# Optimization experiments

Measured on AMD Instinct MI355X. Metric: run time of the kernel, lower is better.

## Reference

```python
import jax, jax.numpy as jnp
import numpy as np

D_MODEL = 1024
NUM_HEADS = 16
DEPTH = D_MODEL // NUM_HEADS  # 64
BATCH, SEQ = 4, 2048


def setup_inputs() -> dict:
    key = jax.random.key(0)
    ks = jax.random.split(key, 9)
    s = 1.0 / np.sqrt(D_MODEL)
    x = jax.random.normal(ks[0], (BATCH, SEQ, D_MODEL), dtype=jnp.float32)
    # Per-head Dense weights stacked on a leading head axis [H, d_model, depth]
    Wq = jax.random.normal(ks[1], (NUM_HEADS, D_MODEL, DEPTH), dtype=jnp.float32) * s
    Wk = jax.random.normal(ks[2], (NUM_HEADS, D_MODEL, DEPTH), dtype=jnp.float32) * s
    Wv = jax.random.normal(ks[3], (NUM_HEADS, D_MODEL, DEPTH), dtype=jnp.float32) * s
    bq = jnp.zeros((NUM_HEADS, DEPTH), dtype=jnp.float32)
    bk = jnp.zeros((NUM_HEADS, DEPTH), dtype=jnp.float32)
    bv = jnp.zeros((NUM_HEADS, DEPTH), dtype=jnp.float32)
    Wo = jax.random.normal(ks[4], (D_MODEL, D_MODEL), dtype=jnp.float32) * s
    bo = jnp.zeros((D_MODEL,), dtype=jnp.float32)
    return {"x": x, "Wq": Wq, "bq": bq, "Wk": Wk, "bk": bk,
            "Wv": Wv, "bv": bv, "Wo": Wo, "bo": bo}


def reference(x, Wq, bq, Wk, bk, Wv, bv, Wo, bo):
    # Batched equivalent of the per-head loop: project, attend, concat heads.
    q = jnp.einsum('bsd,hde->bhse', x, Wq) + bq[:, None, :]  # [B,H,S,depth]
    k = jnp.einsum('bsd,hde->bhse', x, Wk) + bk[:, None, :]
    v = jnp.einsum('bsd,hde->bhse', x, Wv) + bv[:, None, :]
    scale = 1.0 / jnp.sqrt(jnp.asarray(DEPTH, dtype=x.dtype))
    scores = jnp.einsum('bhse,bhte->bhst', q, k) * scale      # [B,H,S,S]
    weights = jax.nn.softmax(scores, axis=-1)
    heads = jnp.einsum('bhst,bhte->bhse', weights, v)         # [B,H,S,depth]
    # concat head outputs along last axis in head order (tf.concat axis=-1)
    multi = jnp.transpose(heads, (0, 2, 1, 3)).reshape(x.shape[0], x.shape[1], D_MODEL)
    return multi @ Wo + bo
```

## Files before the change

kernel.cpp:

```cpp
#include <hip/hip_runtime.h>
#include <hip/hip_bf16.h>

#define BATCH 4
#define SEQ   2048
#define DM    1024
#define NH    16
#define DEPTH 64
#define ROWS  (BATCH*SEQ)
#define NQKV  (3*DM)
#define BH    (BATCH*NH)

typedef __attribute__((ext_vector_type(8))) short bf16x8;
typedef __attribute__((ext_vector_type(4))) float f32x4;
typedef __attribute__((ext_vector_type(16))) float f32x16;
typedef unsigned short u16;
typedef unsigned int   u32;

__device__ __forceinline__ u16 f2bf(float f) {
    union { float f; unsigned u; } v; v.f = f;
    unsigned r = v.u + 0x7fff + ((v.u >> 16) & 1);
    return (u16)(r >> 16);
}

__device__ __forceinline__ u32 pk2bf(float a, float b) {
#if __has_builtin(__builtin_amdgcn_cvt_pk_bf16_f32)
    typedef __attribute__((ext_vector_type(2))) __bf16 v2bf;
    union { v2bf v; u32 u; } u_;
    u_.v = __builtin_amdgcn_cvt_pk_bf16_f32(a, b);
    return u_.u;
#else
    return (u32)f2bf(a) | ((u32)f2bf(b) << 16);
#endif
}

__device__ __forceinline__ void plswap(u32 a, u32 b, u32& x, u32& y) {
#if __has_builtin(__builtin_amdgcn_permlane32_swap)
    typedef __attribute__((ext_vector_type(2))) int i32x2;
    i32x2 r = __builtin_amdgcn_permlane32_swap((int)a, (int)b, false, false);
    x = (u32)r.x; y = (u32)r.y;
#else
    u32 as = (u32)__shfl_xor((int)a, 32);
    u32 bs = (u32)__shfl_xor((int)b, 32);
    int h = (threadIdx.x >> 5) & 1;
    x = h ? bs : a;
    y = h ? b : as;
#endif
}

__device__ __forceinline__ void g2l16(void* lds, const void* g) {
    __builtin_amdgcn_global_load_lds((const __attribute__((address_space(1))) void*)g,
                                     (__attribute__((address_space(3))) void*)lds, 16, 0, 0);
}

__device__ __forceinline__ bf16x8 frag8(const u16* tile, int row, int gl) {
    return *(const bf16x8*)(tile + row * 64 + ((gl ^ (row & 7)) * 8));
}

__device__ __forceinline__ f32x16 mfma32(bf16x8 a, bf16x8 b, f32x16 c) {
    return __builtin_amdgcn_mfma_f32_32x32x16_bf16(a, b, c, 0, 0, 0);
}

__global__ __launch_bounds__(256) void k_prep(const float* __restrict__ x,
                                              const float* __restrict__ Wq, const float* __restrict__ Wk,
                                              const float* __restrict__ Wv, const float* __restrict__ Wo,
                                              u16* __restrict__ xb, u16* __restrict__ BT, u16* __restrict__ WoT) {
    __shared__ u16 T[64][65];
    int tid = threadIdx.x;
    int bx = blockIdx.x;
    if (bx < 2048) {
        int i = bx * 4096 + tid * 4;
        for (int l = 0; l < 4; ++l) {
            float4 v = *(const float4*)(x + i + l * 1024);
            ushort4 o; o.x = f2bf(v.x); o.y = f2bf(v.y); o.z = f2bf(v.z); o.w = f2bf(v.w);
            *(ushort4*)(xb + i + l * 1024) = o;
        }
        return;
    }
    if (bx < 2816) {
        int q = bx - 2048;
        int kt = q & 15, mh = q >> 4, m = mh >> 4, h = mh & 15;
        const float* W = (m == 0) ? Wq : (m == 1) ? Wk : Wv;
        const float* src = W + ((size_t)h * 1024 + kt * 64) * 64;
        int e = tid & 63, r0 = tid >> 6;
        for (int i = 0; i < 16; ++i) { int r = i * 4 + r0; T[r][e] = f2bf(src[r * 64 + e]); }
        __syncthreads();
        int kk = tid & 63, e0 = tid >> 6;
        u16* dst = BT + ((size_t)m * 1024 + h * 64) * 1024 + kt * 64;
        for (int i = 0; i < 16; ++i) { int ee = i * 4 + e0; dst[ee * 1024 + kk] = T[kk][ee]; }
        return;
    }
    {
        int q = bx - 2816;
        int kt = q & 15, nt = q >> 4;
        const float* src = Wo + (size_t)kt * 64 * 1024 + nt * 64;
        int c = tid & 63, r0 = tid >> 6;
        for (int i = 0; i < 16; ++i) { int r = i * 4 + r0; T[r][c] = f2bf(src[r * 1024 + c]); }
        __syncthreads();
        int kk = tid & 63, e0 = tid >> 6;
        u16* dst = WoT + (size_t)nt * 64 * 1024 + kt * 64;
        for (int i = 0; i < 16; ++i) { int ee = i * 4 + e0; dst[ee * 1024 + kk] = T[kk][ee]; }
    }
}

__global__ __launch_bounds__(256, 2) void k_gemm_qkv(const u16* __restrict__ xb, const u16* __restrict__ Wt,
                                                     const float* __restrict__ bq, const float* __restrict__ bk,
                                                     const float* __restrict__ bv,
                                                     u16* __restrict__ Q, u16* __restrict__ K, u16* __restrict__ VT) {
    __shared__ u16 Al[2][128 * 64];
    __shared__ u16 Bl[2][128 * 64];
    int tid = threadIdx.x;
    int wave = tid >> 6, lane = tid & 63, l31 = lane & 31, h2 = lane >> 5;
    int wr = wave >> 1, wc = wave & 1;

    int b = blockIdx.x;
    int wg = (b & 7) * 192 + (b >> 3);

    bool isvt = (wg >= 1024);
    int row0, col0;
    const u16 *Am, *Bm;
    if (!isvt) {
        row0 = (wg >> 4) * 128; col0 = (wg & 15) * 128;
        Am = xb + (size_t)row0 * 1024;
        Bm = Wt + (size_t)col0 * 1024;
    } else {
        int b2 = wg - 1024;
        row0 = (b2 >> 6) * 128; col0 = (b2 & 63) * 128;
        Am = Wt + (size_t)(2048 + row0) * 1024;
        Bm = xb + (size_t)col0 * 1024;
    }

    f32x16 acc[2][2] = {};

    int sr[4], sgs[4], sdst[4];
#pragma unroll
    for (int l = 0; l < 4; ++l) {
        int idx = tid + l * 256;
        sr[l] = idx >> 3; sgs[l] = ((idx & 7) ^ (sr[l] & 7)) * 8; sdst[l] = idx * 8;
    }

#define QKV_STAGE(bufi, k0) \
    { _Pragma("unroll") for (int l = 0; l < 4; ++l) { \
        g2l16(&Al[bufi][sdst[l]], Am + sr[l] * 1024 + (k0) + sgs[l]); \
        g2l16(&Bl[bufi][sdst[l]], Bm + sr[l] * 1024 + (k0) + sgs[l]); } }

#define QKV_COMPUTE(bufi) \
    { _Pragma("unroll") for (int kk = 0; kk < 4; ++kk) { \
        bf16x8 a_[2], bb_[2]; \
        _Pragma("unroll") for (int mi = 0; mi < 2; ++mi) a_[mi] = frag8(Al[bufi], wr * 64 + mi * 32 + l31, 2 * kk + h2); \
        _Pragma("unroll") for (int ni = 0; ni < 2; ++ni) bb_[ni] = frag8(Bl[bufi], wc * 64 + ni * 32 + l31, 2 * kk + h2); \
        _Pragma("unroll") for (int mi = 0; mi < 2; ++mi) \
        _Pragma("unroll") for (int ni = 0; ni < 2; ++ni) \
            acc[mi][ni] = mfma32(a_[mi], bb_[ni], acc[mi][ni]); } }

    QKV_STAGE(0, 0)
    QKV_STAGE(1, 64)

    for (int t = 0; t < 15; ++t) {
        int cur = t & 1;
        asm volatile("s_waitcnt vmcnt(8)" ::: "memory");
        __builtin_amdgcn_s_barrier();
        asm volatile("" ::: "memory");
        __builtin_amdgcn_s_setprio(1);
        QKV_COMPUTE(cur)
        __builtin_amdgcn_s_setprio(0);
        asm volatile("" ::: "memory");
        __builtin_amdgcn_s_barrier();
        if (t < 14) QKV_STAGE(cur, (t + 2) * 64)
    }
    asm volatile("s_waitcnt vmcnt(0)" ::: "memory");
    __builtin_amdgcn_s_barrier();
    asm volatile("" ::: "memory");
    QKV_COMPUTE(1)
#undef QKV_STAGE
#undef QKV_COMPUTE

    if (!isvt) {
        const float QSCALE = 0.125f * 1.4426950408889634f;
        int m = (col0 >= 1024);
        const float* bias = m ? bk : bq;
        u16* dst0 = m ? K : Q;
#pragma unroll
        for (int ni = 0; ni < 2; ++ni) {
            int c = col0 + wc * 64 + ni * 32 + l31;
            int h = (c >> 6) & 15, e = c & 63;
            float bval = bias[h * 64 + e];
#pragma unroll
            for (int mi = 0; mi < 2; ++mi)
#pragma unroll
                for (int reg = 0; reg < 16; ++reg) {
                    int rowg = row0 + wr * 64 + mi * 32 + (reg & 3) + 8 * (reg >> 2) + 4 * h2;
                    int b_ = rowg >> 11, s = rowg & 2047;
                    int bh = b_ * 16 + h;
                    float v = acc[mi][ni][reg] + bval;
                    if (!m) v *= QSCALE;
                    dst0[((size_t)bh * 2048 + s) * 64 + e] = f2bf(v);
                }
        }
    } else {
#pragma unroll
        for (int ni = 0; ni < 2; ++ni) {
            int c = col0 + wc * 64 + ni * 32 + l31;
            int b_ = c >> 11, s = c & 2047;
#pragma unroll
            for (int mi = 0; mi < 2; ++mi)
#pragma unroll
                for (int reg = 0; reg < 16; ++reg) {
                    int ii = row0 + wr * 64 + mi * 32 + (reg & 3) + 8 * (reg >> 2) + 4 * h2;
                    float v = acc[mi][ni][reg] + bv[ii];
                    VT[((size_t)b_ * 1024 + ii) * 2048 + s] = f2bf(v);
                }
        }
    }
}

__global__ __launch_bounds__(256, 4) void k_attn(const u16* __restrict__ Q, const u16* __restrict__ K,
                                                 const u16* __restrict__ VT, u16* __restrict__ A2) {
    __shared__ u16 Kl[2][64 * 64];
    __shared__ u16 Vl[3][64 * 64];
    int tid = threadIdx.x;
    int wave = tid >> 6, lane = tid & 63, l31 = lane & 31, h = lane >> 5;
    int i = blockIdx.x;
    int bh = (i & 7) * 8 + ((i >> 3) & 7);
    int m0 = (i >> 6) * 128;
    const u16* Qb = Q + (size_t)bh * 2048 * 64;
    const u16* Kb = K + (size_t)bh * 2048 * 64;
    const u16* Vb = VT + (size_t)bh * 64 * 2048;

    const u16* kp[2]; const u16* vp[2]; int dsti[2];
    for (int l = 0; l < 2; ++l) {
        int idx = tid + l * 256, r = idx >> 3, gs = ((idx & 7) ^ (r & 7)) * 8;
        dsti[l] = idx * 8;
        kp[l] = Kb + r * 64 + gs;
        vp[l] = Vb + r * 2048 + gs;
    }

    bf16x8 qb[4];
    {
        const u16* q0 = Qb + (size_t)(m0 + wave * 32 + l31) * 64 + h * 8;
#pragma unroll
        for (int s = 0; s < 4; ++s) qb[s] = *(const bf16x8*)(q0 + s * 16);
    }

    for (int l = 0; l < 2; ++l) { g2l16(&Kl[0][dsti[l]], kp[l]); g2l16(&Vl[0][dsti[l]], vp[l]); }
    asm volatile("s_waitcnt vmcnt(0)" ::: "memory");
    __builtin_amdgcn_s_barrier();
    asm volatile("" ::: "memory");

    f32x16 oacc[2] = {};
    float lsum = 0.f;
    bf16x8 pa[4] = {};
    int vw = 1;
    int vr = 2;

    for (int t = 0; t < 32; ++t) {
        int cur = t & 1, nxt = cur ^ 1;

        if (t < 31) {
            for (int l = 0; l < 2; ++l) {
                g2l16(&Kl[nxt][dsti[l]], kp[l] + (t + 1) * 4096);
                g2l16(&Vl[vw][dsti[l]], vp[l] + (t + 1) * 64);
            }
        }

        f32x16 sc[2] = {};
        __builtin_amdgcn_s_setprio(1);
#pragma unroll
        for (int s = 0; s < 4; ++s) {
            bf16x8 kf0 = frag8(Kl[cur], l31,      2 * s + h);
            bf16x8 kf1 = frag8(Kl[cur], 32 + l31, 2 * s + h);
            sc[0] = mfma32(kf0, qb[s], sc[0]);
            sc[1] = mfma32(kf1, qb[s], sc[1]);
        }
        if (t > 0) {
            const u16* vt_ = Vl[vr];
#pragma unroll
            for (int s = 0; s < 4; ++s) {
                bf16x8 bv0 = frag8(vt_, l31,      2 * s + h);
                bf16x8 bv1 = frag8(vt_, 32 + l31, 2 * s + h);
                oacc[0] = mfma32(pa[s], bv0, oacc[0]);
                oacc[1] = mfma32(pa[s], bv1, oacc[1]);
            }
        }
        __builtin_amdgcn_s_setprio(0);

        float sq = 0.f;
#pragma unroll
        for (int kt = 0; kt < 2; ++kt)
#pragma unroll
            for (int gp = 0; gp < 2; ++gp) {
                float e00 = __builtin_amdgcn_exp2f(sc[kt][(2 * gp) * 4 + 0]);
                float e01 = __builtin_amdgcn_exp2f(sc[kt][(2 * gp) * 4 + 1]);
                float e02 = __builtin_amdgcn_exp2f(sc[kt][(2 * gp) * 4 + 2]);
                float e03 = __builtin_amdgcn_exp2f(sc[kt][(2 * gp) * 4 + 3]);
                float e10 = __builtin_amdgcn_exp2f(sc[kt][(2 * gp + 1) * 4 + 0]);
                float e11 = __builtin_amdgcn_exp2f(sc[kt][(2 * gp + 1) * 4 + 1]);
                float e12 = __builtin_amdgcn_exp2f(sc[kt][(2 * gp + 1) * 4 + 2]);
                float e13 = __builtin_amdgcn_exp2f(sc[kt][(2 * gp + 1) * 4 + 3]);
                sq += ((e00 + e01) + (e02 + e03)) + ((e10 + e11) + (e12 + e13));
                u32 ue = pk2bf(e00, e01), ve = pk2bf(e02, e03);
                u32 uo = pk2bf(e10, e11), vo = pk2bf(e12, e13);
                u32 w0, w1, w2, w3;
                plswap(ue, uo, w0, w2);
                plswap(ve, vo, w1, w3);
                union { bf16x8 v; u32 w[4]; } pu;
                pu.w[0] = w0; pu.w[1] = w1; pu.w[2] = w2; pu.w[3] = w3;
                pa[2 * kt + gp] = pu.v;
            }
        lsum += sq;

        if (t < 31) {
            asm volatile("s_waitcnt vmcnt(0)" ::: "memory");
            __builtin_amdgcn_s_barrier();
            asm volatile("" ::: "memory");
        }
        vw = (vw == 2) ? 0 : vw + 1;
        vr = (vr == 2) ? 0 : vr + 1;
    }

#pragma unroll
    for (int s = 0; s < 4; ++s) {
        bf16x8 bv0 = frag8(Vl[1], l31,      2 * s + h);
        bf16x8 bv1 = frag8(Vl[1], 32 + l31, 2 * s + h);
        oacc[0] = mfma32(pa[s], bv0, oacc[0]);
        oacc[1] = mfma32(pa[s], bv1, oacc[1]);
    }

    float linv_own;
    {
        float l2 = lsum + __shfl_xor(lsum, 32);
        linv_own = 1.0f / l2;
    }
    int b_ = bh >> 4, hh = bh & 15;
    for (int g = 0; g < 4; ++g) {
#pragma unroll
        for (int r = 0; r < 4; ++r) {
            float iv = __shfl(linv_own, 8 * g + 4 * h + r);
            int row = b_ * 2048 + m0 + wave * 32 + 8 * g + 4 * h + r;
            for (int dt = 0; dt < 2; ++dt)
                A2[row * 1024 + hh * 64 + dt * 32 + l31] = f2bf(oacc[dt][g * 4 + r] * iv);
        }
    }
}

__global__ __launch_bounds__(256, 2) void k_gemm_out(const u16* __restrict__ A, const u16* __restrict__ BT,
                                                     const float* __restrict__ bo, float* __restrict__ out) {
    __shared__ u16 Al[2][128 * 64];
    __shared__ u16 Bl[2][128 * 64];
    int tid = threadIdx.x;
    int wave = tid >> 6, lane = tid & 63, l31 = lane & 31, h2 = lane >> 5;
    int wr = wave >> 1, wc = wave & 1;

    int b = blockIdx.x;
    int wg = (b & 7) * 64 + (b >> 3);
    int row0 = (wg >> 3) * 128, col0 = (wg & 7) * 128;

    const u16* Am = A  + (size_t)row0 * 1024;
    const u16* Bm = BT + (size_t)col0 * 1024;

    f32x16 acc[2][2] = {};

    int sr[4], sgs[4], sdst[4];
#pragma unroll
    for (int l = 0; l < 4; ++l) {
        int idx = tid + l * 256;
        sr[l] = idx >> 3; sgs[l] = ((idx & 7) ^ (sr[l] & 7)) * 8; sdst[l] = idx * 8;
    }

#define OUT_STAGE(bufi, k0) \
    { _Pragma("unroll") for (int l = 0; l < 4; ++l) { \
        g2l16(&Al[bufi][sdst[l]], Am + sr[l] * 1024 + (k0) + sgs[l]); \
        g2l16(&Bl[bufi][sdst[l]], Bm + sr[l] * 1024 + (k0) + sgs[l]); } }

#define OUT_COMPUTE(bufi) \
    { _Pragma("unroll") for (int kk = 0; kk < 4; ++kk) { \
        bf16x8 a_[2], bb_[2]; \
        _Pragma("unroll") for (int mi = 0; mi < 2; ++mi) a_[mi] = frag8(Al[bufi], wr * 64 + mi * 32 + l31, 2 * kk + h2); \
        _Pragma("unroll") for (int ni = 0; ni < 2; ++ni) bb_[ni] = frag8(Bl[bufi], wc * 64 + ni * 32 + l31, 2 * kk + h2); \
        _Pragma("unroll") for (int mi = 0; mi < 2; ++mi) \
        _Pragma("unroll") for (int ni = 0; ni < 2; ++ni) \
            acc[mi][ni] = mfma32(a_[mi], bb_[ni], acc[mi][ni]); } }

    OUT_STAGE(0, 0)
    OUT_STAGE(1, 64)

    for (int t = 0; t < 15; ++t) {
        int cur = t & 1;
        asm volatile("s_waitcnt vmcnt(8)" ::: "memory");
        __builtin_amdgcn_s_barrier();
        asm volatile("" ::: "memory");
        __builtin_amdgcn_s_setprio(1);
        OUT_COMPUTE(cur)
        __builtin_amdgcn_s_setprio(0);
        asm volatile("" ::: "memory");
        __builtin_amdgcn_s_barrier();
        if (t < 14) OUT_STAGE(cur, (t + 2) * 64)
    }
    asm volatile("s_waitcnt vmcnt(0)" ::: "memory");
    __builtin_amdgcn_s_barrier();
    asm volatile("" ::: "memory");
    OUT_COMPUTE(1)
#undef OUT_STAGE
#undef OUT_COMPUTE

#pragma unroll
    for (int ni = 0; ni < 2; ++ni) {
        int c = col0 + wc * 64 + ni * 32 + l31;
        float bias = bo[c];
#pragma unroll
        for (int mi = 0; mi < 2; ++mi)
#pragma unroll
            for (int reg = 0; reg < 16; ++reg) {
                int rowg = row0 + wr * 64 + mi * 32 + (reg & 3) + 8 * (reg >> 2) + 4 * h2;
                out[(size_t)rowg * 1024 + c] = acc[mi][ni][reg] + bias;
            }
    }
}

extern "C" void kernel_launch(void* const* d_in, const int* in_sizes, int n_in,
                              void* d_out, int out_size, void* d_ws, size_t ws_size,
                              hipStream_t stream) {
    const float* x  = (const float*)d_in[0];
    const float* Wq = (const float*)d_in[1];
    const float* bq = (const float*)d_in[2];
    const float* Wk = (const float*)d_in[3];
    const float* bk = (const float*)d_in[4];
    const float* Wv = (const float*)d_in[5];
    const float* bv = (const float*)d_in[6];
    const float* Wo = (const float*)d_in[7];
    const float* bo = (const float*)d_in[8];
    float* out = (float*)d_out;

    char* ws = (char*)d_ws;
    u16* xb    = (u16*)ws; ws += (size_t)ROWS * DM * 2;
    u16* WqkvT = (u16*)ws; ws += (size_t)NQKV * DM * 2;
    u16* WoT   = (u16*)ws; ws += (size_t)DM * DM * 2;
    u16* Qb    = (u16*)ws; ws += (size_t)BH * SEQ * DEPTH * 2;
    u16* Kb    = (u16*)ws; ws += (size_t)BH * SEQ * DEPTH * 2;
    u16* VTb   = (u16*)ws; ws += (size_t)BH * SEQ * DEPTH * 2;
    u16* A2    = xb;
    (void)ws_size;

    k_prep     <<<dim3(3072),   dim3(256), 0, stream>>>(x, Wq, Wk, Wv, Wo, xb, WqkvT, WoT);
    k_gemm_qkv <<<dim3(1536),   dim3(256), 0, stream>>>(xb, WqkvT, bq, bk, bv, Qb, Kb, VTb);
    k_attn     <<<dim3(1024),   dim3(256), 0, stream>>>(Qb, Kb, VTb, A2);
    k_gemm_out <<<dim3(512),    dim3(256), 0, stream>>>(A2, WoT, bo, out);
}
```

Baseline: 285.5 us.

## Unroll attention loop with static buffer indices and compute row sums via MFMA

Peels the first and last iterations of the attention K/V loop and fully unrolls the middle into six-step bodies, so LDS buffer indices are compile-time constants and the per-iteration branches and modulo-3 counters go away. The softmax denominator is now accumulated by an extra MFMA of the probability fragments against a ones vector, replacing the scalar VALU additions and the cross-lane shuffle at the end. This trades VALU work for one extra MFMA per step (about 50% more PV MFMAs) and sums the bf16-rounded probabilities, which also makes the normalization match the values used for PV. It raises code size and accumulator register pressure.

```diff
diff --git a/kernel.cpp b/kernel.cpp
--- a/kernel.cpp
+++ b/kernel.cpp
@@ -226,12 +226,12 @@
     const u16* Kb = K + (size_t)bh * 2048 * 64;
     const u16* Vb = VT + (size_t)bh * 64 * 2048;
 
-    const u16* kp[2]; const u16* vp[2]; int dsti[2];
+    const u16* kpc[2]; const u16* vpc[2]; int dsti[2];
     for (int l = 0; l < 2; ++l) {
         int idx = tid + l * 256, r = idx >> 3, gs = ((idx & 7) ^ (r & 7)) * 8;
         dsti[l] = idx * 8;
-        kp[l] = Kb + r * 64 + gs;
-        vp[l] = Vb + r * 2048 + gs;
+        kpc[l] = Kb + r * 64 + gs;
+        vpc[l] = Vb + r * 2048 + gs;
     }
 
     bf16x8 qb[4];
@@ -241,80 +241,122 @@
         for (int s = 0; s < 4; ++s) qb[s] = *(const bf16x8*)(q0 + s * 16);
     }
 
-    for (int l = 0; l < 2; ++l) { g2l16(&Kl[0][dsti[l]], kp[l]); g2l16(&Vl[0][dsti[l]], vp[l]); }
+    bf16x8 ones;
+    {
+        union { short s[8]; bf16x8 v; } o_;
+#pragma unroll
+        for (int j = 0; j < 8; ++j) o_.s[j] = (short)0x3F80;
+        ones = o_.v;
+    }
+
+    for (int l = 0; l < 2; ++l) { g2l16(&Kl[0][dsti[l]], kpc[l]); g2l16(&Vl[0][dsti[l]], vpc[l]); }
     asm volatile("s_waitcnt vmcnt(0)" ::: "memory");
     __builtin_amdgcn_s_barrier();
     asm volatile("" ::: "memory");
+    kpc[0] += 4096; kpc[1] += 4096; vpc[0] += 64; vpc[1] += 64;
 
     f32x16 oacc[2] = {};
-    float lsum = 0.f;
-    bf16x8 pa[4] = {};
-    int vw = 1;
-    int vr = 2;
-
-    for (int t = 0; t < 32; ++t) {
-        int cur = t & 1, nxt = cur ^ 1;
-
-        if (t < 31) {
-            for (int l = 0; l < 2; ++l) {
-                g2l16(&Kl[nxt][dsti[l]], kp[l] + (t + 1) * 4096);
-                g2l16(&Vl[vw][dsti[l]], vp[l] + (t + 1) * 64);
-            }
-        }
-
-        f32x16 sc[2] = {};
+    f32x16 lacc = {};
+    bf16x8 pa[4];
+
+#define ATT_EXP(sc0_, sc1_) \
+    { _Pragma("unroll") for (int kt = 0; kt < 2; ++kt) { \
+        const f32x16& s_ = kt ? (sc1_) : (sc0_); \
+        _Pragma("unroll") for (int gp = 0; gp < 2; ++gp) { \
+            float e00 = __builtin_amdgcn_exp2f(s_[(2 * gp) * 4 + 0]); \
+            float e01 = __builtin_amdgcn_exp2f(s_[(2 * gp) * 4 + 1]); \
+            float e02 = __builtin_amdgcn_exp2f(s_[(2 * gp) * 4 + 2]); \
+            float e03 = __builtin_amdgcn_exp2f(s_[(2 * gp) * 4 + 3]); \
+            float e10 = __builtin_amdgcn_exp2f(s_[(2 * gp + 1) * 4 + 0]); \
+            float e11 = __builtin_amdgcn_exp2f(s_[(2 * gp + 1) * 4 + 1]); \
+            float e12 = __builtin_amdgcn_exp2f(s_[(2 * gp + 1) * 4 + 2]); \
+            float e13 = __builtin_amdgcn_exp2f(s_[(2 * gp + 1) * 4 + 3]); \
+            u32 ue = pk2bf(e00, e01), ve = pk2bf(e02, e03); \
+            u32 uo = pk2bf(e10, e11), vo = pk2bf(e12, e13); \
+            u32 w0, w1, w2, w3; \
+            plswap(ue, uo, w0, w2); \
+            plswap(ve, vo, w1, w3); \
+            union { bf16x8 v; u32 w[4]; } pu; \
+            pu.w[0] = w0; pu.w[1] = w1; pu.w[2] = w2; pu.w[3] = w3; \
+            pa[2 * kt + gp] = pu.v; \
+        } } }
+
+#define ATT_BODY(KS, KN, VW, VR) \
+    { \
+        g2l16(&Kl[KN][dsti[0]], kpc[0]); g2l16(&Vl[VW][dsti[0]], vpc[0]); \
+        g2l16(&Kl[KN][dsti[1]], kpc[1]); g2l16(&Vl[VW][dsti[1]], vpc[1]); \
+        f32x16 sc0 = {}, sc1 = {}; \
+        __builtin_amdgcn_s_setprio(1); \
+        _Pragma("unroll") for (int s = 0; s < 4; ++s) { \
+            bf16x8 kf0 = frag8(Kl[KS], l31,      2 * s + h); \
+            bf16x8 kf1 = frag8(Kl[KS], 32 + l31, 2 * s + h); \
+            sc0 = mfma32(kf0, qb[s], sc0); \
+            sc1 = mfma32(kf1, qb[s], sc1); \
+        } \
+        _Pragma("unroll") for (int s = 0; s < 4; ++s) { \
+            bf16x8 bv0 = frag8(Vl[VR], l31,      2 * s + h); \
+            bf16x8 bv1 = frag8(Vl[VR], 32 + l31, 2 * s + h); \
+            oacc[0] = mfma32(pa[s], bv0, oacc[0]); \
+            oacc[1] = mfma32(pa[s], bv1, oacc[1]); \
+            lacc    = mfma32(pa[s], ones, lacc); \
+        } \
+        __builtin_amdgcn_s_setprio(0); \
+        ATT_EXP(sc0, sc1) \
+        asm volatile("s_waitcnt vmcnt(0)" ::: "memory"); \
+        __builtin_amdgcn_s_barrier(); \
+        asm volatile("" ::: "memory"); \
+        kpc[0] += 4096; kpc[1] += 4096; vpc[0] += 64; vpc[1] += 64; \
+    }
+
+    {
+        g2l16(&Kl[1][dsti[0]], kpc[0]); g2l16(&Vl[1][dsti[0]], vpc[0]);
+        g2l16(&Kl[1][dsti[1]], kpc[1]); g2l16(&Vl[1][dsti[1]], vpc[1]);
+        f32x16 sc0 = {}, sc1 = {};
         __builtin_amdgcn_s_setprio(1);
 #pragma unroll
         for (int s = 0; s < 4; ++s) {
-            bf16x8 kf0 = frag8(Kl[cur], l31,      2 * s + h);
-            bf16x8 kf1 = frag8(Kl[cur], 32 + l31, 2 * s + h);
-            sc[0] = mfma32(kf0, qb[s], sc[0]);
-            sc[1] = mfma32(kf1, qb[s], sc[1]);
-        }
-        if (t > 0) {
-            const u16* vt_ = Vl[vr];
-#pragma unroll
-            for (int s = 0; s < 4; ++s) {
-                bf16x8 bv0 = frag8(vt_, l31,      2 * s + h);
-                bf16x8 bv1 = frag8(vt_, 32 + l31, 2 * s + h);
-                oacc[0] = mfma32(pa[s], bv0, oacc[0]);
-                oacc[1] = mfma32(pa[s], bv1, oacc[1]);
-            }
+            bf16x8 kf0 = frag8(Kl[0], l31,      2 * s + h);
+            bf16x8 kf1 = frag8(Kl[0], 32 + l31, 2 * s + h);
+            sc0 = mfma32(kf0, qb[s], sc0);
+            sc1 = mfma32(kf1, qb[s], sc1);
         }
         __builtin_amdgcn_s_setprio(0);
-
-        float sq = 0.f;
-#pragma unroll
-        for (int kt = 0; kt < 2; ++kt)
-#pragma unroll
-            for (int gp = 0; gp < 2; ++gp) {
-                float e00 = __builtin_amdgcn_exp2f(sc[kt][(2 * gp) * 4 + 0]);
-                float e01 = __builtin_amdgcn_exp2f(sc[kt][(2 * gp) * 4 + 1]);
-                float e02 = __builtin_amdgcn_exp2f(sc[kt][(2 * gp) * 4 + 2]);
-                float e03 = __builtin_amdgcn_exp2f(sc[kt][(2 * gp) * 4 + 3]);
-                float e10 = __builtin_amdgcn_exp2f(sc[kt][(2 * gp + 1) * 4 + 0]);
-                float e11 = __builtin_amdgcn_exp2f(sc[kt][(2 * gp + 1) * 4 + 1]);
-                float e12 = __builtin_amdgcn_exp2f(sc[kt][(2 * gp + 1) * 4 + 2]);
-                float e13 = __builtin_amdgcn_exp2f(sc[kt][(2 * gp + 1) * 4 + 3]);
-                sq += ((e00 + e01) + (e02 + e03)) + ((e10 + e11) + (e12 + e13));
-                u32 ue = pk2bf(e00, e01), ve = pk2bf(e02, e03);
-                u32 uo = pk2bf(e10, e11), vo = pk2bf(e12, e13);
-                u32 w0, w1, w2, w3;
-                plswap(ue, uo, w0, w2);
-                plswap(ve, vo, w1, w3);
-                union { bf16x8 v; u32 w[4]; } pu;
-                pu.w[0] = w0; pu.w[1] = w1; pu.w[2] = w2; pu.w[3] = w3;
-                pa[2 * kt + gp] = pu.v;
-            }
-        lsum += sq;
-
-        if (t < 31) {
-            asm volatile("s_waitcnt vmcnt(0)" ::: "memory");
-            __builtin_amdgcn_s_barrier();
-            asm volatile("" ::: "memory");
-        }
-        vw = (vw == 2) ? 0 : vw + 1;
-        vr = (vr == 2) ? 0 : vr + 1;
+        ATT_EXP(sc0, sc1)
+        asm volatile("s_waitcnt vmcnt(0)" ::: "memory");
+        __builtin_amdgcn_s_barrier();
+        asm volatile("" ::: "memory");
+        kpc[0] += 4096; kpc[1] += 4096; vpc[0] += 64; vpc[1] += 64;
+    }
+
+    for (int u = 0; u < 5; ++u) {
+        ATT_BODY(1, 0, 2, 0)
+        ATT_BODY(0, 1, 0, 1)
+        ATT_BODY(1, 0, 1, 2)
+        ATT_BODY(0, 1, 2, 0)
+        ATT_BODY(1, 0, 0, 1)
+        ATT_BODY(0, 1, 1, 2)
+    }
+
+    {
+        f32x16 sc0 = {}, sc1 = {};
+        __builtin_amdgcn_s_setprio(1);
+#pragma unroll
+        for (int s = 0; s < 4; ++s) {
+            bf16x8 kf0 = frag8(Kl[1], l31,      2 * s + h);
+            bf16x8 kf1 = frag8(Kl[1], 32 + l31, 2 * s + h);
+            sc0 = mfma32(kf0, qb[s], sc0);
+            sc1 = mfma32(kf1, qb[s], sc1);
+        }
+#pragma unroll
+        for (int s = 0; s < 4; ++s) {
+            bf16x8 bv0 = frag8(Vl[0], l31,      2 * s + h);
+            bf16x8 bv1 = frag8(Vl[0], 32 + l31, 2 * s + h);
+            oacc[0] = mfma32(pa[s], bv0, oacc[0]);
+            oacc[1] = mfma32(pa[s], bv1, oacc[1]);
+            lacc    = mfma32(pa[s], ones, lacc);
+        }
+        __builtin_amdgcn_s_setprio(0);
+        ATT_EXP(sc0, sc1)
     }
 
 #pragma unroll
@@ -323,18 +365,16 @@
         bf16x8 bv1 = frag8(Vl[1], 32 + l31, 2 * s + h);
         oacc[0] = mfma32(pa[s], bv0, oacc[0]);
         oacc[1] = mfma32(pa[s], bv1, oacc[1]);
-    }
-
-    float linv_own;
-    {
-        float l2 = lsum + __shfl_xor(lsum, 32);
-        linv_own = 1.0f / l2;
-    }
+        lacc    = mfma32(pa[s], ones, lacc);
+    }
+#undef ATT_BODY
+#undef ATT_EXP
+
     int b_ = bh >> 4, hh = bh & 15;
     for (int g = 0; g < 4; ++g) {
 #pragma unroll
         for (int r = 0; r < 4; ++r) {
-            float iv = __shfl(linv_own, 8 * g + 4 * h + r);
+            float iv = 1.0f / lacc[g * 4 + r];
             int row = b_ * 2048 + m0 + wave * 32 + 8 * g + 4 * h + r;
             for (int dt = 0; dt < 2; ++dt)
                 A2[row * 1024 + hh * 64 + dt * 32 + l31] = f2bf(oacc[dt][g * 4 + r] * iv);
```

Measured after the change: 581.0 us. +103.5%, slower.

## Enlarge QKV and output GEMM tiles to 256x128 with 512-thread blocks

Applied to the files above, without the earlier changes.

Both projection GEMMs move from 128x128 tiles with 4 waves to 256x128 tiles with 8 waves. Each B tile staged in LDS is now reused across twice as many rows, and the grid is halved. The A and B staging loads are split into separate loops, and the vmcnt wait is adjusted for the new count of in-flight loads per stage. The cost is double-buffered LDS growing to about 96 KB per block, which may cut the number of resident blocks per CU and reduce latency hiding.

```diff
diff --git a/kernel.cpp b/kernel.cpp
--- a/kernel.cpp
+++ b/kernel.cpp
@@ -102,62 +102,71 @@
     }
 }
 
-__global__ __launch_bounds__(256, 2) void k_gemm_qkv(const u16* __restrict__ xb, const u16* __restrict__ Wt,
+__global__ __launch_bounds__(512, 2) void k_gemm_qkv(const u16* __restrict__ xb, const u16* __restrict__ Wt,
                                                      const float* __restrict__ bq, const float* __restrict__ bk,
                                                      const float* __restrict__ bv,
                                                      u16* __restrict__ Q, u16* __restrict__ K, u16* __restrict__ VT) {
-    __shared__ u16 Al[2][128 * 64];
+    __shared__ u16 Al[2][256 * 64];
     __shared__ u16 Bl[2][128 * 64];
     int tid = threadIdx.x;
     int wave = tid >> 6, lane = tid & 63, l31 = lane & 31, h2 = lane >> 5;
     int wr = wave >> 1, wc = wave & 1;
 
     int b = blockIdx.x;
-    int wg = (b & 7) * 192 + (b >> 3);
-
-    bool isvt = (wg >= 1024);
+    int wg = (b & 7) * 96 + (b >> 3);
+
+    bool isvt = (wg >= 512);
     int row0, col0;
     const u16 *Am, *Bm;
     if (!isvt) {
-        row0 = (wg >> 4) * 128; col0 = (wg & 15) * 128;
+        row0 = (wg >> 4) * 256; col0 = (wg & 15) * 128;
         Am = xb + (size_t)row0 * 1024;
         Bm = Wt + (size_t)col0 * 1024;
     } else {
-        int b2 = wg - 1024;
-        row0 = (b2 >> 6) * 128; col0 = (b2 & 63) * 128;
+        int b2 = wg - 512;
+        row0 = (b2 >> 6) * 256; col0 = (b2 & 63) * 128;
         Am = Wt + (size_t)(2048 + row0) * 1024;
         Bm = xb + (size_t)col0 * 1024;
     }
 
     f32x16 acc[2][2] = {};
 
-    int sr[4], sgs[4], sdst[4];
+    int srA[4], sgsA[4], sdstA[4];
 #pragma unroll
     for (int l = 0; l < 4; ++l) {
-        int idx = tid + l * 256;
-        sr[l] = idx >> 3; sgs[l] = ((idx & 7) ^ (sr[l] & 7)) * 8; sdst[l] = idx * 8;
+        int idx = tid + l * 512;
+        srA[l] = idx >> 3; sgsA[l] = ((idx & 7) ^ (srA[l] & 7)) * 8; sdstA[l] = idx * 8;
+    }
+    int srB[2], sgsB[2], sdstB[2];
+#pragma unroll
+    for (int l = 0; l < 2; ++l) {
+        int idx = tid + l * 512;
+        srB[l] = idx >> 3; sgsB[l] = ((idx & 7) ^ (srB[l] & 7)) * 8; sdstB[l] = idx * 8;
     }
 
 #define QKV_STAGE(bufi, k0) \
-    { _Pragma("unroll") for (int l = 0; l < 4; ++l) { \
-        g2l16(&Al[bufi][sdst[l]], Am + sr[l] * 1024 + (k0) + sgs[l]); \
-        g2l16(&Bl[bufi][sdst[l]], Bm + sr[l] * 1024 + (k0) + sgs[l]); } }
+    { _Pragma("unroll") for (int l = 0; l < 4; ++l) \
+        g2l16(&Al[bufi][sdstA[l]], Am + srA[l] * 1024 + (k0) + sgsA[l]); \
+      _Pragma("unroll") for (int l = 0; l < 2; ++l) \
+        g2l16(&Bl[bufi][sdstB[l]], Bm + srB[l] * 1024 + (k0) + sgsB[l]); }
 
 #define QKV_COMPUTE(bufi) \
     { _Pragma("unroll") for (int kk = 0; kk < 4; ++kk) { \
-        bf16x8 a_[2], bb_[2]; \
-        _Pragma("unroll") for (int mi = 0; mi < 2; ++mi) a_[mi] = frag8(Al[bufi], wr * 64 + mi * 32 + l31, 2 * kk + h2); \
-        _Pragma("unroll") for (int ni = 0; ni < 2; ++ni) bb_[ni] = frag8(Bl[bufi], wc * 64 + ni * 32 + l31, 2 * kk + h2); \
-        _Pragma("unroll") for (int mi = 0; mi < 2; ++mi) \
-        _Pragma("unroll") for (int ni = 0; ni < 2; ++ni) \
-            acc[mi][ni] = mfma32(a_[mi], bb_[ni], acc[mi][ni]); } }
+        bf16x8 a0_ = frag8(Al[bufi], wr * 64 + l31,      2 * kk + h2); \
+        bf16x8 a1_ = frag8(Al[bufi], wr * 64 + 32 + l31, 2 * kk + h2); \
+        bf16x8 b0_ = frag8(Bl[bufi], wc * 64 + l31,      2 * kk + h2); \
+        bf16x8 b1_ = frag8(Bl[bufi], wc * 64 + 32 + l31, 2 * kk + h2); \
+        acc[0][0] = mfma32(a0_, b0_, acc[0][0]); \
+        acc[0][1] = mfma32(a0_, b1_, acc[0][1]); \
+        acc[1][0] = mfma32(a1_, b0_, acc[1][0]); \
+        acc[1][1] = mfma32(a1_, b1_, acc[1][1]); } }
 
     QKV_STAGE(0, 0)
     QKV_STAGE(1, 64)
 
     for (int t = 0; t < 15; ++t) {
         int cur = t & 1;
-        asm volatile("s_waitcnt vmcnt(8)" ::: "memory");
+        asm volatile("s_waitcnt vmcnt(6)" ::: "memory");
         __builtin_amdgcn_s_barrier();
         asm volatile("" ::: "memory");
         __builtin_amdgcn_s_setprio(1);
@@ -342,50 +351,59 @@
     }
 }
 
-__global__ __launch_bounds__(256, 2) void k_gemm_out(const u16* __restrict__ A, const u16* __restrict__ BT,
+__global__ __launch_bounds__(512, 2) void k_gemm_out(const u16* __restrict__ A, const u16* __restrict__ BT,
                                                      const float* __restrict__ bo, float* __restrict__ out) {
-    __shared__ u16 Al[2][128 * 64];
+    __shared__ u16 Al[2][256 * 64];
     __shared__ u16 Bl[2][128 * 64];
     int tid = threadIdx.x;
     int wave = tid >> 6, lane = tid & 63, l31 = lane & 31, h2 = lane >> 5;
     int wr = wave >> 1, wc = wave & 1;
 
     int b = blockIdx.x;
-    int wg = (b & 7) * 64 + (b >> 3);
-    int row0 = (wg >> 3) * 128, col0 = (wg & 7) * 128;
+    int wg = (b & 7) * 32 + (b >> 3);
+    int row0 = (wg >> 3) * 256, col0 = (wg & 7) * 128;
 
     const u16* Am = A  + (size_t)row0 * 1024;
     const u16* Bm = BT + (size_t)col0 * 1024;
 
     f32x16 acc[2][2] = {};
 
-    int sr[4], sgs[4], sdst[4];
+    int srA[4], sgsA[4], sdstA[4];
 #pragma unroll
     for (int l = 0; l < 4; ++l) {
-        int idx = tid + l * 256;
-        sr[l] = idx >> 3; sgs[l] = ((idx & 7) ^ (sr[l] & 7)) * 8; sdst[l] = idx * 8;
+        int idx = tid + l * 512;
+        srA[l] = idx >> 3; sgsA[l] = ((idx & 7) ^ (srA[l] & 7)) * 8; sdstA[l] = idx * 8;
+    }
+    int srB[2], sgsB[2], sdstB[2];
+#pragma unroll
+    for (int l = 0; l < 2; ++l) {
+        int idx = tid + l * 512;
+        srB[l] = idx >> 3; sgsB[l] = ((idx & 7) ^ (srB[l] & 7)) * 8; sdstB[l] = idx * 8;
     }
 
 #define OUT_STAGE(bufi, k0) \
-    { _Pragma("unroll") for (int l = 0; l < 4; ++l) { \
-        g2l16(&Al[bufi][sdst[l]], Am + sr[l] * 1024 + (k0) + sgs[l]); \
-        g2l16(&Bl[bufi][sdst[l]], Bm + sr[l] * 1024 + (k0) + sgs[l]); } }
+    { _Pragma("unroll") for (int l = 0; l < 4; ++l) \
+        g2l16(&Al[bufi][sdstA[l]], Am + srA[l] * 1024 + (k0) + sgsA[l]); \
+      _Pragma("unroll") for (int l = 0; l < 2; ++l) \
+        g2l16(&Bl[bufi][sdstB[l]], Bm + srB[l] * 1024 + (k0) + sgsB[l]); }
 
 #define OUT_COMPUTE(bufi) \
     { _Pragma("unroll") for (int kk = 0; kk < 4; ++kk) { \
-        bf16x8 a_[2], bb_[2]; \
-        _Pragma("unroll") for (int mi = 0; mi < 2; ++mi) a_[mi] = frag8(Al[bufi], wr * 64 + mi * 32 + l31, 2 * kk + h2); \
-        _Pragma("unroll") for (int ni = 0; ni < 2; ++ni) bb_[ni] = frag8(Bl[bufi], wc * 64 + ni * 32 + l31, 2 * kk + h2); \
-        _Pragma("unroll") for (int mi = 0; mi < 2; ++mi) \
-        _Pragma("unroll") for (int ni = 0; ni < 2; ++ni) \
-            acc[mi][ni] = mfma32(a_[mi], bb_[ni], acc[mi][ni]); } }
+        bf16x8 a0_ = frag8(Al[bufi], wr * 64 + l31,      2 * kk + h2); \
+        bf16x8 a1_ = frag8(Al[bufi], wr * 64 + 32 + l31, 2 * kk + h2); \
+        bf16x8 b0_ = frag8(Bl[bufi], wc * 64 + l31,      2 * kk + h2); \
+        bf16x8 b1_ = frag8(Bl[bufi], wc * 64 + 32 + l31, 2 * kk + h2); \
+        acc[0][0] = mfma32(a0_, b0_, acc[0][0]); \
+        acc[0][1] = mfma32(a0_, b1_, acc[0][1]); \
+        acc[1][0] = mfma32(a1_, b0_, acc[1][0]); \
+        acc[1][1] = mfma32(a1_, b1_, acc[1][1]); } }
 
     OUT_STAGE(0, 0)
     OUT_STAGE(1, 64)
 
     for (int t = 0; t < 15; ++t) {
         int cur = t & 1;
-        asm volatile("s_waitcnt vmcnt(8)" ::: "memory");
+        asm volatile("s_waitcnt vmcnt(6)" ::: "memory");
         __builtin_amdgcn_s_barrier();
         asm volatile("" ::: "memory");
         __builtin_amdgcn_s_setprio(1);
@@ -441,7 +459,7 @@
     (void)ws_size;
 
     k_prep     <<<dim3(3072),   dim3(256), 0, stream>>>(x, Wq, Wk, Wv, Wo, xb, WqkvT, WoT);
-    k_gemm_qkv <<<dim3(1536),   dim3(256), 0, stream>>>(xb, WqkvT, bq, bk, bv, Qb, Kb, VTb);
+    k_gemm_qkv <<<dim3(768),    dim3(512), 0, stream>>>(xb, WqkvT, bq, bk, bv, Qb, Kb, VTb);
     k_attn     <<<dim3(1024),   dim3(256), 0, stream>>>(Qb, Kb, VTb, A2);
-    k_gemm_out <<<dim3(512),    dim3(256), 0, stream>>>(A2, WoT, bo, out);
-}
+    k_gemm_out <<<dim3(256),    dim3(512), 0, stream>>>(A2, WoT, bo, out);
+}
```

Measured after the change: 276.9 us, median of 2. -3.0%, faster.
